# Kernel optimization log

Hardware: AMD Instinct MI355X
Metric: run time of the kernel (lower is better)

The kernel has to match this reference:

```python
import jax, jax.numpy as jnp
import numpy as np

EPS = 1e-8
SMALL = 1e-3


def _skew(v):
    # v: [B,3] -> [B,3,3]
    vx, vy, vz = v[:, 0], v[:, 1], v[:, 2]
    z = jnp.zeros_like(vx)
    row0 = jnp.stack([z, -vz, vy], axis=-1)
    row1 = jnp.stack([vz, z, -vx], axis=-1)
    row2 = jnp.stack([-vy, vx, z], axis=-1)
    return jnp.stack([row0, row1, row2], axis=-2)


def rotmat_axis_angle_stable(aa):
    # aa: [B,3] axis*angle -> [B,3,3], Taylor-stable near theta=0
    theta = jnp.linalg.norm(aa, axis=1)
    theta2 = theta * theta + EPS
    A = jnp.sin(theta) / (theta + EPS)
    Bc = (1.0 - jnp.cos(theta)) / theta2
    th2 = theta * theta
    th4 = th2 * th2
    small = theta < SMALL
    A = jnp.where(small, 1.0 - th2 / 6.0 + th4 / 120.0, A)
    Bc = jnp.where(small, 0.5 - th2 / 24.0 + th4 / 720.0, Bc)
    K = _skew(aa)
    I = jnp.eye(3, dtype=aa.dtype)
    return I + A[:, None, None] * K + Bc[:, None, None] * jnp.matmul(K, K)


def _euler_to_rot(rpy):
    # rpy: [J,3] -> [J,3,3] (URDF origin rotations, constants)
    r, p, y = rpy[:, 0], rpy[:, 1], rpy[:, 2]
    cr, sr = jnp.cos(r), jnp.sin(r)
    cp, sp = jnp.cos(p), jnp.sin(p)
    cy, sy = jnp.cos(y), jnp.sin(y)
    row0 = jnp.stack([cy * cp, cy * sp * sr - sy * cr, cy * sp * cr + sy * sr], -1)
    row1 = jnp.stack([sy * cp, sy * sp * sr + cy * cr, sy * sp * cr - cy * sr], -1)
    row2 = jnp.stack([-sp, cp * sr, cp * cr], -1)
    return jnp.stack([row0, row1, row2], axis=-2)


def setup_inputs() -> dict:
    key = jax.random.key(0)
    k1, k2, k3, k4 = jax.random.split(key, 4)
    B, J = 131072, 24
    joint_angles = jax.random.normal(k1, (B, J), dtype=jnp.float32)
    # URDF origin constants: small offsets + rotations per joint
    xyz = 0.1 * jax.random.normal(k2, (J, 3), dtype=jnp.float32)
    rpy = 0.3 * jax.random.normal(k3, (J, 3), dtype=jnp.float32)
    R = _euler_to_rot(rpy)                                      # [J,3,3]
    T_origins = jnp.tile(jnp.eye(4, dtype=jnp.float32), (J, 1, 1))
    T_origins = T_origins.at[:, :3, :3].set(R).at[:, :3, 3].set(xyz)
    ax = jax.random.normal(k4, (J, 3), dtype=jnp.float32)
    axes = ax / jnp.linalg.norm(ax, axis=1, keepdims=True)      # unit axes
    return {"joint_angles": joint_angles, "T_origins": T_origins, "axes": axes}


def reference(joint_angles, T_origins, axes) -> jnp.ndarray:
    # joint_angles: [B,J]; T_origins: [J,4,4]; axes: [J,3]
    joint_angles = joint_angles.astype(jnp.float32)
    B = joint_angles.shape[0]
    eye4 = jnp.eye(4, dtype=jnp.float32)

    def step(T_parent, xs):
        T_org, axis, ang = xs                     # [4,4], [3], [B]
        aa = axis[None, :] * ang[:, None]         # [B,3]
        Rj = rotmat_axis_angle_stable(aa)         # [B,3,3]
        Tj = jnp.broadcast_to(eye4, (B, 4, 4)).at[:, :3, :3].set(Rj)
        T_child = jnp.matmul(jnp.matmul(T_parent, T_org), Tj)   # [B,4,4]
        return T_child, T_child[:, :3, 3]

    T0 = jnp.broadcast_to(eye4, (B, 4, 4))
    xs = (T_origins, axes, joint_angles.T)        # scan over J joints
    _, pos = jax.lax.scan(step, T0, xs)           # pos: [J,B,3]
    base_pos = jnp.zeros((B, 3), dtype=jnp.float32)
    pos = jnp.transpose(pos, (1, 0, 2)).reshape(B, -1)          # [B,J*3]
    return jnp.concatenate([base_pos, pos], axis=1)             # [B,(J+1)*3]
```

## Files before the change

### kernel.cpp

```cpp
#include <hip/hip_runtime.h>

#define BLK 256
#define NJ 24
#define G 8
#define NG (NJ / G)

__global__ __launch_bounds__(BLK, 2)
void fk_kernel(const float* __restrict__ angles,
               const float* __restrict__ Torg,
               const float* __restrict__ axes,
               float* __restrict__ out,
               int B)
{
    __shared__ float stage[BLK * 75];
    __shared__ float sQK[NJ * 8];
    __shared__ float sAx[NJ * 4];

    const int tid = threadIdx.x;

    if (tid < NJ) {
        const float* o = Torg + tid * 16;
        const float m00=o[0], m01=o[1], m02=o[2];
        const float m10=o[4], m11=o[5], m12=o[6];
        const float m20=o[8], m21=o[9], m22=o[10];
        const float tr = m00 + m11 + m22;
        float qw, qx, qy, qz;
        if (tr > 0.f) {
            const float S = sqrtf(tr + 1.f) * 2.f;
            qw = 0.25f * S;
            qx = (m21 - m12) / S;
            qy = (m02 - m20) / S;
            qz = (m10 - m01) / S;
        } else if (m00 > m11 && m00 > m22) {
            const float S = sqrtf(1.f + m00 - m11 - m22) * 2.f;
            qw = (m21 - m12) / S;
            qx = 0.25f * S;
            qy = (m01 + m10) / S;
            qz = (m02 + m20) / S;
        } else if (m11 > m22) {
            const float S = sqrtf(1.f + m11 - m00 - m22) * 2.f;
            qw = (m02 - m20) / S;
            qx = (m01 + m10) / S;
            qy = 0.25f * S;
            qz = (m12 + m21) / S;
        } else {
            const float S = sqrtf(1.f + m22 - m00 - m11) * 2.f;
            qw = (m10 - m01) / S;
            qx = (m02 + m20) / S;
            qy = (m12 + m21) / S;
            qz = 0.25f * S;
        }
        float* q = &sQK[tid * 8];
        q[0] = qw; q[1] = qx; q[2] = qy; q[3] = qz;
        q[4] = o[3]; q[5] = o[7]; q[6] = o[11]; q[7] = 0.f;
        float* ax = &sAx[tid * 4];
        ax[0] = axes[tid*3+0]; ax[1] = axes[tid*3+1]; ax[2] = axes[tid*3+2]; ax[3] = 0.f;
    }
    __syncthreads();

    const int b = blockIdx.x * BLK + tid;
    const float4* ap = reinterpret_cast<const float4*>(angles + (size_t)b * NJ);

    float Qw = 1.f, Qx = 0.f, Qy = 0.f, Qz = 0.f;
    float tx = 0.f, ty = 0.f, tz = 0.f;

    float* srow = &stage[tid * 75];
    srow[0] = 0.f; srow[1] = 0.f; srow[2] = 0.f;

    float4 av0 = ap[0], av1 = ap[1];

    #pragma unroll 1
    for (int g = 0; g < NG; ++g) {
        float4 nv0, nv1;
        if (g + 1 < NG) { nv0 = ap[2*g + 2]; nv1 = ap[2*g + 3]; }

        float a[G];
        a[0]=av0.x; a[1]=av0.y; a[2]=av0.z; a[3]=av0.w;
        a[4]=av1.x; a[5]=av1.y; a[6]=av1.z; a[7]=av1.w;

        float U[G][4];
        float OT[G][3];
        #pragma unroll
        for (int u = 0; u < G; ++u) {
            const int j = g * G + u;
            const float4 qo = *reinterpret_cast<const float4*>(&sQK[j*8]);
            const float4 ot = *reinterpret_cast<const float4*>(&sQK[j*8+4]);
            const float4 ax = *reinterpret_cast<const float4*>(&sAx[j*4]);
            OT[u][0] = ot.x; OT[u][1] = ot.y; OT[u][2] = ot.z;

            const float h = 0.5f * a[u];
            const float s = __sinf(h);
            const float c = __cosf(h);
            const float bx = s * ax.x, by = s * ax.y, bz = s * ax.z;

            U[u][0] = qo.x*c  - qo.y*bx - qo.z*by - qo.w*bz;
            U[u][1] = qo.x*bx + qo.y*c  + qo.z*bz - qo.w*by;
            U[u][2] = qo.x*by - qo.y*bz + qo.z*c  + qo.w*bx;
            U[u][3] = qo.x*bz + qo.y*by - qo.z*bx + qo.w*c;
        }

        #pragma unroll
        for (int u = 0; u < G; ++u) {
            const int j = g * G + u;
            const float ox = OT[u][0], oy = OT[u][1], oz = OT[u][2];

            const float cx = Qy*oz - Qz*oy + Qw*ox;
            const float cy = Qz*ox - Qx*oz + Qw*oy;
            const float cz = Qx*oy - Qy*ox + Qw*oz;
            const float dx = Qy*cz - Qz*cy;
            const float dy = Qz*cx - Qx*cz;
            const float dz = Qx*cy - Qy*cx;
            tx = tx + ox + 2.f*dx;
            ty = ty + oy + 2.f*dy;
            tz = tz + oz + 2.f*dz;

            const float uw = U[u][0], ux = U[u][1], uy = U[u][2], uz = U[u][3];
            const float nw = Qw*uw - Qx*ux - Qy*uy - Qz*uz;
            const float nx = Qw*ux + Qx*uw + Qy*uz - Qz*uy;
            const float ny = Qw*uy - Qx*uz + Qy*uw + Qz*ux;
            const float nz = Qw*uz + Qx*uy - Qy*ux + Qz*uw;
            Qw = nw; Qx = nx; Qy = ny; Qz = nz;

            srow[3 + 3*j + 0] = tx;
            srow[3 + 3*j + 1] = ty;
            srow[3 + 3*j + 2] = tz;
        }

        av0 = nv0; av1 = nv1;
    }

    __syncthreads();

    float4* out4 = reinterpret_cast<float4*>(out + (size_t)blockIdx.x * BLK * 75);
    const float4* st4 = reinterpret_cast<const float4*>(stage);
    #pragma unroll 1
    for (int i = tid; i < BLK * 75 / 4; i += BLK) {
        out4[i] = st4[i];
    }
}

extern "C" void kernel_launch(void* const* d_in, const int* in_sizes, int n_in,
                              void* d_out, int out_size, void* d_ws, size_t ws_size,
                              hipStream_t stream) {
    const float* angles = (const float*)d_in[0];
    const float* Torg   = (const float*)d_in[1];
    const float* axes   = (const float*)d_in[2];
    float* out = (float*)d_out;

    const int B = in_sizes[0] / NJ;
    const int grid = (B + BLK - 1) / BLK;

    fk_kernel<<<grid, BLK, 0, stream>>>(angles, Torg, axes, out, B);
}
```

Baseline: 22.14 us.

## Precompute joint constants in a prep kernel and read them from global memory

Moves the per-block quaternion conversion of the origin transforms into a separate single-block prep kernel that writes a packed constant table to the workspace. The main kernel then reads joint constants with uniform global loads, which can become scalar loads, instead of computing them per block and syncing through shared memory. The block size is also halved to 128, so the staging buffer shrinks and more blocks can be resident. The cost is an extra kernel launch and a dependency between the two kernels.

```diff
diff --git a/kernel.cpp b/kernel.cpp
--- a/kernel.cpp
+++ b/kernel.cpp
@@ -1,63 +1,62 @@
 #include <hip/hip_runtime.h>
 
-#define BLK 256
+#define BLK 128
 #define NJ 24
 #define G 8
 #define NG (NJ / G)
 
+__global__ void fk_prep(const float* __restrict__ Torg,
+                        const float* __restrict__ axes,
+                        float* __restrict__ cst)
+{
+    const int j = threadIdx.x;
+    if (j >= NJ) return;
+    const float* o = Torg + j * 16;
+    const float m00=o[0], m01=o[1], m02=o[2];
+    const float m10=o[4], m11=o[5], m12=o[6];
+    const float m20=o[8], m21=o[9], m22=o[10];
+    const float tr = m00 + m11 + m22;
+    float qw, qx, qy, qz;
+    if (tr > 0.f) {
+        const float S = sqrtf(tr + 1.f) * 2.f;
+        qw = 0.25f * S;
+        qx = (m21 - m12) / S;
+        qy = (m02 - m20) / S;
+        qz = (m10 - m01) / S;
+    } else if (m00 > m11 && m00 > m22) {
+        const float S = sqrtf(1.f + m00 - m11 - m22) * 2.f;
+        qw = (m21 - m12) / S;
+        qx = 0.25f * S;
+        qy = (m01 + m10) / S;
+        qz = (m02 + m20) / S;
+    } else if (m11 > m22) {
+        const float S = sqrtf(1.f + m11 - m00 - m22) * 2.f;
+        qw = (m02 - m20) / S;
+        qx = (m01 + m10) / S;
+        qy = 0.25f * S;
+        qz = (m12 + m21) / S;
+    } else {
+        const float S = sqrtf(1.f + m22 - m00 - m11) * 2.f;
+        qw = (m10 - m01) / S;
+        qx = (m02 + m20) / S;
+        qy = (m12 + m21) / S;
+        qz = 0.25f * S;
+    }
+    float* c = cst + j * 12;
+    c[0] = qw; c[1] = qx; c[2] = qy; c[3] = qz;
+    c[4] = axes[j*3+0]; c[5] = axes[j*3+1]; c[6] = axes[j*3+2]; c[7] = 0.f;
+    c[8] = o[3]; c[9] = o[7]; c[10] = o[11]; c[11] = 0.f;
+}
+
 __global__ __launch_bounds__(BLK, 2)
 void fk_kernel(const float* __restrict__ angles,
-               const float* __restrict__ Torg,
-               const float* __restrict__ axes,
+               const float* __restrict__ cst,
                float* __restrict__ out,
                int B)
 {
     __shared__ float stage[BLK * 75];
-    __shared__ float sQK[NJ * 8];
-    __shared__ float sAx[NJ * 4];
 
     const int tid = threadIdx.x;
-
-    if (tid < NJ) {
-        const float* o = Torg + tid * 16;
-        const float m00=o[0], m01=o[1], m02=o[2];
-        const float m10=o[4], m11=o[5], m12=o[6];
-        const float m20=o[8], m21=o[9], m22=o[10];
-        const float tr = m00 + m11 + m22;
-        float qw, qx, qy, qz;
-        if (tr > 0.f) {
-            const float S = sqrtf(tr + 1.f) * 2.f;
-            qw = 0.25f * S;
-            qx = (m21 - m12) / S;
-            qy = (m02 - m20) / S;
-            qz = (m10 - m01) / S;
-        } else if (m00 > m11 && m00 > m22) {
-            const float S = sqrtf(1.f + m00 - m11 - m22) * 2.f;
-            qw = (m21 - m12) / S;
-            qx = 0.25f * S;
-            qy = (m01 + m10) / S;
-            qz = (m02 + m20) / S;
-        } else if (m11 > m22) {
-            const float S = sqrtf(1.f + m11 - m00 - m22) * 2.f;
-            qw = (m02 - m20) / S;
-            qx = (m01 + m10) / S;
-            qy = 0.25f * S;
-            qz = (m12 + m21) / S;
-        } else {
-            const float S = sqrtf(1.f + m22 - m00 - m11) * 2.f;
-            qw = (m10 - m01) / S;
-            qx = (m02 + m20) / S;
-            qy = (m12 + m21) / S;
-            qz = 0.25f * S;
-        }
-        float* q = &sQK[tid * 8];
-        q[0] = qw; q[1] = qx; q[2] = qy; q[3] = qz;
-        q[4] = o[3]; q[5] = o[7]; q[6] = o[11]; q[7] = 0.f;
-        float* ax = &sAx[tid * 4];
-        ax[0] = axes[tid*3+0]; ax[1] = axes[tid*3+1]; ax[2] = axes[tid*3+2]; ax[3] = 0.f;
-    }
-    __syncthreads();
-
     const int b = blockIdx.x * BLK + tid;
     const float4* ap = reinterpret_cast<const float4*>(angles + (size_t)b * NJ);
 
@@ -83,20 +82,20 @@
         #pragma unroll
         for (int u = 0; u < G; ++u) {
             const int j = g * G + u;
-            const float4 qo = *reinterpret_cast<const float4*>(&sQK[j*8]);
-            const float4 ot = *reinterpret_cast<const float4*>(&sQK[j*8+4]);
-            const float4 ax = *reinterpret_cast<const float4*>(&sAx[j*4]);
-            OT[u][0] = ot.x; OT[u][1] = ot.y; OT[u][2] = ot.z;
+            const float qow = cst[j*12+0], qox = cst[j*12+1];
+            const float qoy = cst[j*12+2], qoz = cst[j*12+3];
+            const float axx = cst[j*12+4], axy = cst[j*12+5], axz = cst[j*12+6];
+            OT[u][0] = cst[j*12+8]; OT[u][1] = cst[j*12+9]; OT[u][2] = cst[j*12+10];
 
             const float h = 0.5f * a[u];
             const float s = __sinf(h);
             const float c = __cosf(h);
-            const float bx = s * ax.x, by = s * ax.y, bz = s * ax.z;
+            const float bx = s * axx, by = s * axy, bz = s * axz;
 
-            U[u][0] = qo.x*c  - qo.y*bx - qo.z*by - qo.w*bz;
-            U[u][1] = qo.x*bx + qo.y*c  + qo.z*bz - qo.w*by;
-            U[u][2] = qo.x*by - qo.y*bz + qo.z*c  + qo.w*bx;
-            U[u][3] = qo.x*bz + qo.y*by - qo.z*bx + qo.w*c;
+            U[u][0] = qow*c  - qox*bx - qoy*by - qoz*bz;
+            U[u][1] = qow*bx + qox*c  + qoy*bz - qoz*by;
+            U[u][2] = qow*by - qox*bz + qoy*c  + qoz*bx;
+            U[u][3] = qow*bz + qox*by - qoy*bx + qoz*c;
         }
 
         #pragma unroll
@@ -146,9 +145,11 @@
     const float* Torg   = (const float*)d_in[1];
     const float* axes   = (const float*)d_in[2];
     float* out = (float*)d_out;
+    float* cst = (float*)d_ws;
 
     const int B = in_sizes[0] / NJ;
     const int grid = (B + BLK - 1) / BLK;
 
-    fk_kernel<<<grid, BLK, 0, stream>>>(angles, Torg, axes, out, B);
+    fk_prep<<<1, 64, 0, stream>>>(Torg, axes, cst);
+    fk_kernel<<<grid, BLK, 0, stream>>>(angles, cst, out, B);
 }
```

New measurement: 27.00 us. 1.22x slower.
